# Performance work log

Measured on AMD Instinct MI355X. Metric: run time of the kernel, lower is better.

## Reference

```python
import jax, jax.numpy as jnp
import numpy as np

T, B = 80, 256                 # timesteps (max objs per image), num sequences (images)
OBJ_DIM, EMBED, HID = 4096, 200, 512
NCLS = 151                      # 150 VG classes + background
D = HID + OBJ_DIM + EMBED + 128 # decoder inputs_dim = 4936


def _packed_gather_idx():
    # descending lengths 80..41, mimicking a sorted PackedSequence
    lengths = np.array([T - (i * 40) // B for i in range(B)])
    idx = []
    for t in range(T):
        bs = int((lengths > t).sum())
        idx.extend(t * B + b for b in range(bs))
    return np.asarray(idx, dtype=np.int32)  # [15504]


def setup_inputs() -> dict:
    key = jax.random.key(0)
    ks = jax.random.split(key, 6)
    s = jnp.float32(0.02)
    return {
        "sequence": jax.random.normal(ks[0], (T, B, D), jnp.float32),
        "embed": jax.random.normal(ks[1], (NCLS + 1, EMBED), jnp.float32) * s,
        "W_in": jax.random.normal(ks[2], (6 * HID, D + EMBED), jnp.float32) * s,
        "b_in": jnp.zeros((6 * HID,), jnp.float32),
        "W_state": jax.random.normal(ks[3], (5 * HID, HID), jnp.float32) * s,
        "b_state": jnp.zeros((5 * HID,), jnp.float32),
        "W_out": jax.random.normal(ks[4], (NCLS, HID), jnp.float32) * s,
        "b_out": jnp.zeros((NCLS,), jnp.float32),
        "gather_idx": jnp.asarray(_packed_gather_idx()),
    }


def reference(sequence, embed, W_in, b_in, W_state, b_state, W_out, b_out, gather_idx):
    H = HID

    def step(carry, x_t):
        h, c, prev_embed = carry
        ti = jnp.concatenate([x_t, prev_embed], axis=1)          # [B, D+E]
        pi = ti @ W_in.T + b_in                                   # [B, 6H]
        ps = h @ W_state.T + b_state                              # [B, 5H]
        i_g = jax.nn.sigmoid(pi[:, 0*H:1*H] + ps[:, 0*H:1*H])
        f_g = jax.nn.sigmoid(pi[:, 1*H:2*H] + ps[:, 1*H:2*H])
        m_i = jnp.tanh(pi[:, 2*H:3*H] + ps[:, 2*H:3*H])
        o_g = jax.nn.sigmoid(pi[:, 3*H:4*H] + ps[:, 3*H:4*H])
        c_new = i_g * m_i + f_g * c
        out = o_g * jnp.tanh(c_new)
        hw_g = jax.nn.sigmoid(pi[:, 4*H:5*H] + ps[:, 4*H:5*H])
        h_new = hw_g * out + (1.0 - hw_g) * pi[:, 5*H:6*H]        # highway
        pred = h_new @ W_out.T + b_out                            # [B, NCLS]
        # softmax is monotonic: argmax of softmax(pred)[:,1:] == argmax of pred[:,1:]
        best = jnp.argmax(pred[:, 1:], axis=1) + 1                # [B], in [1, NCLS-1]
        pe_new = embed[best + 1]                                  # [B, E]
        return (h_new, c_new, pe_new), (pred, best)

    h0 = jnp.zeros((B, HID), sequence.dtype)
    c0 = jnp.zeros((B, HID), sequence.dtype)
    pe0 = jnp.broadcast_to(embed[0], (B, EMBED))                  # 'start' token embed
    _, (dists, commits) = jax.lax.scan(step, (h0, c0, pe0), sequence)
    # packed (timestep-major) flattening of valid entries only
    out_dists = dists.reshape(T * B, NCLS)[gather_idx]            # [N, NCLS]
    out_commits = commits.reshape(T * B)[gather_idx]              # [N]
    return out_dists, out_commits
```

## Files before the change

### kernel.cpp

```cpp
#include <hip/hip_runtime.h>
#include <cstddef>
#include <cstdint>

#define T_STEPS 80
#define BATCH   256
#define DIM     4936
#define EMB     200
#define DE      5136
#define HID     512
#define SIXH    3072
#define FIVEH   2560
#define NCLS    151
#define NPACK   15504
#define NKT     156
#define NKT_H   16
#define NCOMB   2816
#define BUF2SZ  32768
#define PSBUF   32768

typedef unsigned short ushort_t;
typedef short short8 __attribute__((ext_vector_type(8)));
typedef float f32x4 __attribute__((ext_vector_type(4)));
typedef float f32x16 __attribute__((ext_vector_type(16)));

__device__ inline ushort_t f2bf_rn(float x) {
    union { float f; uint32_t u; } v; v.f = x;
    uint32_t u = v.u;
    return (ushort_t)((u + 0x7FFFu + ((u >> 16) & 1u)) >> 16);
}
__device__ inline float bf2f(ushort_t b) {
    union { float f; uint32_t u; } v; v.u = ((uint32_t)b) << 16;
    return v.f;
}
__device__ inline float sigmoidf(float x) { return 1.f / (1.f + expf(-x)); }

__global__ __launch_bounds__(256) void convert_split(
    const float* __restrict__ src, int ld, int kvalid,
    ushort_t* __restrict__ hi, ushort_t* __restrict__ lo, int nktiles)
{
    __shared__ float s[128][33];
    const int tid = threadIdx.x;
    const int kt  = blockIdx.x;
    const int mt  = blockIdx.y;

#pragma unroll
    for (int it = 0; it < 4; ++it) {
        int idx = it * 256 + tid;
        int row = idx >> 3;
        int f4  = idx & 7;
        int k   = kt * 32 + f4 * 4;
        const float* p = src + (size_t)(mt * 128 + row) * ld + k;
        float4 v;
        if (k + 3 < kvalid) v = *(const float4*)p;
        else {
            v.x = (k + 0) < kvalid ? p[0] : 0.f;
            v.y = (k + 1) < kvalid ? p[1] : 0.f;
            v.z = (k + 2) < kvalid ? p[2] : 0.f;
            v.w = (k + 3) < kvalid ? p[3] : 0.f;
        }
        s[row][f4 * 4 + 0] = v.x; s[row][f4 * 4 + 1] = v.y;
        s[row][f4 * 4 + 2] = v.z; s[row][f4 * 4 + 3] = v.w;
    }
    __syncthreads();

    const size_t base = ((size_t)mt * nktiles + kt) * 4096;
#pragma unroll
    for (int it = 0; it < 2; ++it) {
        int o   = it * 256 + tid;
        int kb  = o >> 7;
        int row = o & 127;
        alignas(16) ushort_t hbuf[8];
        alignas(16) ushort_t lbuf[8];
#pragma unroll
        for (int e = 0; e < 8; ++e) {
            float x = s[row][kb * 8 + e];
            ushort_t hh = f2bf_rn(x);
            float lof = x - bf2f(hh);
            hbuf[e] = hh;
            lbuf[e] = f2bf_rn(lof);
        }
        *(uint4*)(hi + base + (size_t)o * 8) = *(const uint4*)hbuf;
        *(uint4*)(lo + base + (size_t)o * 8) = *(const uint4*)lbuf;
    }
}

__device__ inline void gload16(const ushort_t* g, ushort_t* l) {
    __builtin_amdgcn_global_load_lds(
        (const __attribute__((address_space(1))) void*)g,
        (__attribute__((address_space(3))) void*)l, 16, 0, 0);
}

__global__ __launch_bounds__(512, 1) void mfma3(
    const ushort_t* __restrict__ Ah, const ushort_t* __restrict__ Al,
    const ushort_t* __restrict__ Bh, const ushort_t* __restrict__ Bl,
    const float* __restrict__ bias, float* __restrict__ OUT,
    int nkt, int ldout, int nt)
{
    extern __shared__ __align__(16) ushort_t smem[];

    const int tid  = threadIdx.x;
    const int wave = tid >> 6;
    const int lane = tid & 63;

    int mtb, ntb;
    {
        const int L = blockIdx.x;
        if ((nt & 7) == 0) {
            const int x = L & 7;
            const int s = L >> 3;
            mtb = x + 8 * (s / 12);
            ntb = s % 12;
        } else {
            mtb = L / 12;
            ntb = L % 12;
        }
    }
    const int wr = wave >> 2;
    const int wc = wave & 3;

    f32x16 acc[4][2];
#pragma unroll
    for (int i = 0; i < 4; ++i)
#pragma unroll
        for (int j = 0; j < 2; ++j)
#pragma unroll
            for (int r = 0; r < 16; ++r) acc[i][j][r] = 0.f;

    const size_t a0 = (size_t)(2 * mtb) * nkt * 4096;
    const size_t a1 = a0 + (size_t)nkt * 4096;
    const size_t b0 = (size_t)(2 * ntb) * nkt * 4096;
    const size_t b1 = b0 + (size_t)nkt * 4096;

#define STAGE2(slot, kt_) do {                                      \
        ushort_t* d = smem + (slot) * BUF2SZ;                       \
        const size_t ko = (size_t)(kt_) * 4096 + tid * 8;           \
        gload16(Ah + a0 + ko, d + tid * 8);                         \
        gload16(Ah + a1 + ko, d + 4096 + tid * 8);                  \
        gload16(Al + a0 + ko, d + 8192 + tid * 8);                  \
        gload16(Al + a1 + ko, d + 12288 + tid * 8);                 \
        gload16(Bh + b0 + ko, d + 16384 + tid * 8);                 \
        gload16(Bh + b1 + ko, d + 20480 + tid * 8);                 \
        gload16(Bl + b0 + ko, d + 24576 + tid * 8);                 \
        gload16(Bl + b1 + ko, d + 28672 + tid * 8);                 \
    } while (0)

    const int lrow = lane & 31;
    const int kg   = lane >> 5;
    const int aBase = wr * 4096;
    const int bBase = 16384 + (wc >> 1) * 4096;
    const int bCol  = (wc & 1) * 64;

    STAGE2(0, 0);

    for (int kt = 0; kt < nkt; ++kt) {
        asm volatile("s_waitcnt vmcnt(0)" ::: "memory");
        __builtin_amdgcn_sched_barrier(0);
        __builtin_amdgcn_s_barrier();
        if (kt + 1 < nkt) STAGE2((kt + 1) & 1, kt + 1);

        const ushort_t* p = smem + (kt & 1) * BUF2SZ;
#pragma unroll
        for (int kh = 0; kh < 2; ++kh) {
            const int ko = (kh * 2 + kg) * 1024;
            short8 a_h[4], a_l[4], b_h[2], b_l[2];
#pragma unroll
            for (int ms = 0; ms < 4; ++ms) {
                const int ao = aBase + ko + (ms * 32 + lrow) * 8;
                a_h[ms] = *(const short8*)&p[ao];
                a_l[ms] = *(const short8*)&p[8192 + ao];
            }
#pragma unroll
            for (int ns = 0; ns < 2; ++ns) {
                const int bo = bBase + ko + (bCol + ns * 32 + lrow) * 8;
                b_h[ns] = *(const short8*)&p[bo];
                b_l[ns] = *(const short8*)&p[8192 + bo];
            }
#pragma unroll
            for (int ms = 0; ms < 4; ++ms)
#pragma unroll
                for (int ns = 0; ns < 2; ++ns) {
                    acc[ms][ns] = __builtin_amdgcn_mfma_f32_32x32x16_bf16(a_h[ms], b_h[ns], acc[ms][ns], 0, 0, 0);
                    acc[ms][ns] = __builtin_amdgcn_mfma_f32_32x32x16_bf16(a_h[ms], b_l[ns], acc[ms][ns], 0, 0, 0);
                    acc[ms][ns] = __builtin_amdgcn_mfma_f32_32x32x16_bf16(a_l[ms], b_h[ns], acc[ms][ns], 0, 0, 0);
                }
        }
    }
#undef STAGE2

#pragma unroll
    for (int ms = 0; ms < 4; ++ms)
#pragma unroll
        for (int ns = 0; ns < 2; ++ns) {
            const int col = ntb * 256 + wc * 64 + ns * 32 + (lane & 31);
            const float bv = bias[col];
            const int rowb = mtb * 256 + wr * 128 + ms * 32 + 4 * (lane >> 5);
#pragma unroll
            for (int r = 0; r < 16; ++r) {
                const int row = rowb + (r & 3) + 8 * (r >> 2);
                OUT[(size_t)row * ldout + col] = acc[ms][ns][r] + bv;
            }
        }
}

__global__ __launch_bounds__(256, 1) void ps_full(
    const ushort_t* __restrict__ hH, const ushort_t* __restrict__ hL,
    const ushort_t* __restrict__ WcH, const ushort_t* __restrict__ WcL,
    const float* __restrict__ bias_comb,
    float* __restrict__ psF)
{
    extern __shared__ __align__(16) ushort_t psmem[];

    const int tid  = threadIdx.x;
    const int wave = tid >> 6;
    const int lane = tid & 63;
    const int ntile = blockIdx.x;
    const int mtile = blockIdx.y;
    const int amt = mtile >> 1, arh = mtile & 1;
    const int bmt = ntile >> 1, brh = ntile & 1;
    const int wr = wave >> 1, wc = wave & 1;

    f32x4 acc[2][2];
#pragma unroll
    for (int i = 0; i < 2; ++i)
#pragma unroll
        for (int j = 0; j < 2; ++j) acc[i][j] = (f32x4){0.f, 0.f, 0.f, 0.f};

    const int lw    = wave * 512;
    const int lsrcA = wave * 1024 + arh * 512 + lane * 8;
    const int lsrcB = wave * 1024 + brh * 512 + lane * 8;
    const int kb = lane >> 4;
    const int lr = lane & 15;

#define STAGE_PS(slot, r_) do {                                           \
        ushort_t* d = psmem + (slot) * PSBUF;                             \
        _Pragma("unroll")                                                 \
        for (int ki_ = 0; ki_ < 4; ++ki_) {                               \
            const int kt_ = (r_) * 4 + ki_;                               \
            const size_t at_ = ((size_t)(amt * NKT_H + kt_)) * 4096;      \
            const size_t bt_ = ((size_t)(bmt * NKT_H + kt_)) * 4096;      \
            gload16(hH  + at_ + lsrcA, d + ki_ * 2048 + lw);              \
            gload16(hL  + at_ + lsrcA, d + 8192 + ki_ * 2048 + lw);       \
            gload16(WcH + bt_ + lsrcB, d + 16384 + ki_ * 2048 + lw);      \
            gload16(WcL + bt_ + lsrcB, d + 24576 + ki_ * 2048 + lw);      \
        }                                                                 \
    } while (0)

    STAGE_PS(0, 0);

    for (int r = 0; r < 4; ++r) {
        asm volatile("s_waitcnt vmcnt(0)" ::: "memory");
        __builtin_amdgcn_sched_barrier(0);
        __builtin_amdgcn_s_barrier();
        if (r + 1 < 4) STAGE_PS((r + 1) & 1, r + 1);

        const ushort_t* p = psmem + (r & 1) * PSBUF;
#pragma unroll
        for (int ki = 0; ki < 4; ++ki) {
            short8 ah[2], al[2], bh[2], bl[2];
#pragma unroll
            for (int i = 0; i < 2; ++i) {
                const int ao = ki * 2048 + kb * 512 + (wr * 32 + i * 16 + lr) * 8;
                ah[i] = *(const short8*)&p[ao];
                al[i] = *(const short8*)&p[8192 + ao];
            }
#pragma unroll
            for (int j = 0; j < 2; ++j) {
                const int bo = ki * 2048 + kb * 512 + (wc * 32 + j * 16 + lr) * 8;
                bh[j] = *(const short8*)&p[16384 + bo];
                bl[j] = *(const short8*)&p[24576 + bo];
            }
#pragma unroll
            for (int i = 0; i < 2; ++i)
#pragma unroll
                for (int j = 0; j < 2; ++j) {
                    acc[i][j] = __builtin_amdgcn_mfma_f32_16x16x32_bf16(ah[i], bh[j], acc[i][j], 0, 0, 0);
                    acc[i][j] = __builtin_amdgcn_mfma_f32_16x16x32_bf16(ah[i], bl[j], acc[i][j], 0, 0, 0);
                    acc[i][j] = __builtin_amdgcn_mfma_f32_16x16x32_bf16(al[i], bh[j], acc[i][j], 0, 0, 0);
                }
        }
    }
#undef STAGE_PS

    float* out = psF + (size_t)(mtile * 64) * NCOMB + ntile * 64;
#pragma unroll
    for (int i = 0; i < 2; ++i) {
        const int row = wr * 32 + i * 16 + (lane >> 4) * 4;
#pragma unroll
        for (int j = 0; j < 2; ++j) {
            const int col = wc * 32 + j * 16 + (lane & 15);
            const float bv = bias_comb[ntile * 64 + col];
#pragma unroll
            for (int r = 0; r < 4; ++r)
                out[(size_t)(row + r) * NCOMB + col] = acc[i][j][r] + bv;
        }
    }
}

__global__ __launch_bounds__(256) void ew_gemm(
    const float* __restrict__ embed, const float* __restrict__ Win,
    float* __restrict__ EW)
{
    __shared__ float As[16][68];
    __shared__ float Bs[16][68];
    const int tid = threadIdx.x;
    const int tx  = tid & 15;
    const int ty  = tid >> 4;
    const int n0  = blockIdx.x * 64;
    const int m0  = blockIdx.y * 64;
    const int lrow = tid >> 2;
    const int lk   = (tid & 3) * 4;

    float acc[4][4];
#pragma unroll
    for (int i = 0; i < 4; ++i)
#pragma unroll
        for (int j = 0; j < 4; ++j) acc[i][j] = 0.f;

    for (int k0 = 0; k0 < EMB; k0 += 16) {
        int k = k0 + lk;
        float4 av = {0.f,0.f,0.f,0.f}, bv = {0.f,0.f,0.f,0.f};
        if (k < EMB) {
            int am = m0 + lrow;
            if (am < 152) av = *(const float4*)(embed + (size_t)am * EMB + k);
            bv = *(const float4*)(Win + (size_t)(n0 + lrow) * DE + DIM + k);
        }
        __syncthreads();
        As[lk + 0][lrow] = av.x; As[lk + 1][lrow] = av.y;
        As[lk + 2][lrow] = av.z; As[lk + 3][lrow] = av.w;
        Bs[lk + 0][lrow] = bv.x; Bs[lk + 1][lrow] = bv.y;
        Bs[lk + 2][lrow] = bv.z; Bs[lk + 3][lrow] = bv.w;
        __syncthreads();
#pragma unroll
        for (int kk = 0; kk < 16; ++kk) {
            float4 a4 = *(const float4*)&As[kk][ty * 4];
            float4 b4 = *(const float4*)&Bs[kk][tx * 4];
            float avr[4] = {a4.x, a4.y, a4.z, a4.w};
            float bvr[4] = {b4.x, b4.y, b4.z, b4.w};
#pragma unroll
            for (int i = 0; i < 4; ++i)
#pragma unroll
                for (int j = 0; j < 4; ++j)
                    acc[i][j] = fmaf(avr[i], bvr[j], acc[i][j]);
        }
    }
#pragma unroll
    for (int i = 0; i < 4; ++i) {
        int m = m0 + ty * 4 + i;
        if (m < 152) {
#pragma unroll
            for (int j = 0; j < 4; ++j)
                EW[(size_t)m * SIXH + n0 + tx * 4 + j] = acc[i][j];
        }
    }
}

__global__ __launch_bounds__(256) void prep_misc(
    const float* __restrict__ Wout, const float* __restrict__ b_state,
    const float* __restrict__ b_out,
    float* __restrict__ padW, float* __restrict__ bc)
{
    int i = blockIdx.x * 256 + threadIdx.x;
    if (i < 256 * 512) {
        int row = i >> 9;
        padW[i] = (row < NCLS) ? Wout[i] : 0.f;
    }
    if (i < NCOMB) {
        float v;
        if (i < FIVEH)                 v = b_state[i];
        else if (i - FIVEH < NCLS)     v = b_out[i - FIVEH];
        else                           v = 0.f;
        bc[i] = v;
    }
}

__global__ __launch_bounds__(256) void init_state(
    float* __restrict__ c, ushort_t* __restrict__ hHt, ushort_t* __restrict__ hLt)
{
    int i = blockIdx.x * 256 + threadIdx.x;
    if (i < BATCH * HID) { c[i] = 0.f; hHt[i] = 0; hLt[i] = 0; }
}

__global__ __launch_bounds__(256) void step_fused(
    const float* __restrict__ px_t,
    const float* __restrict__ EW,
    const float* __restrict__ psF,
    int first,
    ushort_t* __restrict__ hHt, ushort_t* __restrict__ hLt,
    float* __restrict__ c, float* __restrict__ hF,
    float* __restrict__ dists_prev,
    int*   __restrict__ commit_prev)
{
    __shared__ float hs[HID];
    __shared__ float preds_s[NCLS + 1];
    __shared__ int   commit_sh;

    const int tid = threadIdx.x;
    const int b   = blockIdx.x;

    const float* px = px_t + (size_t)b * SIXH;
    const float* pp = psF + (size_t)b * NCOMB;

    float pxv[2][6], ppv[2][5], cv[2];
#pragma unroll
    for (int it = 0; it < 2; ++it) {
        const int u = it * 256 + tid;
#pragma unroll
        for (int k2 = 0; k2 < 5; ++k2) {
            pxv[it][k2] = px[k2 * HID + u];
            ppv[it][k2] = pp[k2 * HID + u];
        }
        pxv[it][5] = px[5 * HID + u];
        cv[it] = c[(size_t)b * HID + u];
    }

    int erow = 0;
    if (!first) {
        if (tid < NCLS) {
            float pr = pp[2560 + tid];
            preds_s[tid] = pr;
            dists_prev[(size_t)b * NCLS + tid] = pr;
        }
        __syncthreads();
        if (tid < 64) {
            float bv = -__builtin_inff();
            int   bi = NCLS;
            for (int n = 1 + tid; n < NCLS; n += 64) {
                float v = preds_s[n];
                if (v > bv) { bv = v; bi = n; }
            }
#pragma unroll
            for (int off = 32; off; off >>= 1) {
                float ov = __shfl_down(bv, off);
                int   oi = __shfl_down(bi, off);
                if (ov > bv || (ov == bv && oi < bi)) { bv = ov; bi = oi; }
            }
            if (tid == 0) {
                commit_prev[b] = bi;
                commit_sh = bi;
            }
        }
        __syncthreads();
        erow = commit_sh + 1;
    }

    const float* ew = EW + (size_t)erow * SIXH;

#pragma unroll
    for (int it = 0; it < 2; ++it) {
        const int u = it * 256 + tid;
        float p[6];
#pragma unroll
        for (int k2 = 0; k2 < 5; ++k2)
            p[k2] = pxv[it][k2] + ew[k2 * HID + u] + ppv[it][k2];
        p[5] = pxv[it][5] + ew[5 * HID + u];

        float i_g = sigmoidf(p[0]);
        float f_g = sigmoidf(p[1]);
        float m_i = tanhf(p[2]);
        float o_g = sigmoidf(p[3]);
        float c_new = i_g * m_i + f_g * cv[it];
        float outv  = o_g * tanhf(c_new);
        float hw    = sigmoidf(p[4]);
        float h_new = hw * outv + (1.f - hw) * p[5];
        c[(size_t)b * HID + u]  = c_new;
        hF[(size_t)b * HID + u] = h_new;
        hs[u] = h_new;
    }
    __syncthreads();

    if (tid < 128) {
        const int half = tid >> 6;
        const int ch   = tid & 63;
        const int mt   = b >> 7;
        const int row  = b & 127;
        const size_t off = ((size_t)(mt * NKT_H + (ch >> 2))) * 4096
                         + (size_t)(ch & 3) * 1024 + (size_t)row * 8;
        alignas(16) ushort_t buf[8];
        if (half == 0) {
#pragma unroll
            for (int e = 0; e < 8; ++e) buf[e] = f2bf_rn(hs[ch * 8 + e]);
            *(uint4*)(hHt + off) = *(const uint4*)buf;
        } else {
#pragma unroll
            for (int e = 0; e < 8; ++e) {
                float x = hs[ch * 8 + e];
                buf[e] = f2bf_rn(x - bf2f(f2bf_rn(x)));
            }
            *(uint4*)(hLt + off) = *(const uint4*)buf;
        }
    }
}

__global__ __launch_bounds__(192) void finalize_last(
    const float* __restrict__ hF, const float* __restrict__ Wout,
    const float* __restrict__ b_out,
    float* __restrict__ dists_last, int* __restrict__ commits_last)
{
    __shared__ float hsh[HID];
    __shared__ float preds[NCLS + 1];
    const int b = blockIdx.x;
    const int tid = threadIdx.x;

    if (tid < 128) {
        float4 v = *(const float4*)(hF + (size_t)b * HID + tid * 4);
        *(float4*)&hsh[tid * 4] = v;
    }
    __syncthreads();
    if (tid < NCLS) {
        const float* w = Wout + (size_t)tid * HID;
        float s0 = 0.f, s1 = 0.f, s2 = 0.f, s3 = 0.f;
        for (int k = 0; k < HID; k += 4) {
            float4 w4 = *(const float4*)(w + k);
            float4 h4 = *(const float4*)&hsh[k];
            s0 = fmaf(h4.x, w4.x, s0);
            s1 = fmaf(h4.y, w4.y, s1);
            s2 = fmaf(h4.z, w4.z, s2);
            s3 = fmaf(h4.w, w4.w, s3);
        }
        float s = b_out[tid] + ((s0 + s1) + (s2 + s3));
        preds[tid] = s;
        dists_last[(size_t)b * NCLS + tid] = s;
    }
    __syncthreads();
    if (tid == 0) {
        int bi = 1; float bv = preds[1];
        for (int n = 2; n < NCLS; ++n) {
            float v = preds[n];
            if (v > bv) { bv = v; bi = n; }
        }
        commits_last[b] = bi;
    }
}

__global__ __launch_bounds__(192) void gather_out(
    const float* __restrict__ dists, const int* __restrict__ commits,
    const int* __restrict__ gidx, float* __restrict__ out)
{
    const int i = blockIdx.x;
    const int g = gidx[i];
    if (threadIdx.x < NCLS)
        out[(size_t)i * NCLS + threadIdx.x] = dists[(size_t)g * NCLS + threadIdx.x];
    if (threadIdx.x == NCLS)
        out[(size_t)NPACK * NCLS + i] = (float)commits[g];
}

extern "C" void kernel_launch(void* const* d_in, const int* in_sizes, int n_in,
                              void* d_out, int out_size, void* d_ws, size_t ws_size,
                              hipStream_t stream)
{
    const float* X      = (const float*)d_in[0];
    const float* embed  = (const float*)d_in[1];
    const float* Win    = (const float*)d_in[2];
    const float* b_in   = (const float*)d_in[3];
    const float* Wst    = (const float*)d_in[4];
    const float* b_st   = (const float*)d_in[5];
    const float* Wout   = (const float*)d_in[6];
    const float* b_out  = (const float*)d_in[7];
    const int*   gidx   = (const int*)d_in[8];

    hipFuncSetAttribute((const void*)mfma3,
                        hipFuncAttributeMaxDynamicSharedMemorySize,
                        2 * BUF2SZ * 2);
    hipFuncSetAttribute((const void*)ps_full,
                        hipFuncAttributeMaxDynamicSharedMemorySize,
                        2 * PSBUF * 2);

    const size_t WN  = (size_t)24 * NKT * 4096;
    const size_t WCN = (size_t)22 * NKT_H * 4096;
    const size_t HN  = (size_t)2 * NKT_H * 4096;

    ushort_t* Wh  = (ushort_t*)d_ws;
    ushort_t* Wl  = Wh + WN;
    ushort_t* WcH = Wl + WN;
    ushort_t* WcL = WcH + WCN;
    ushort_t* hHt = WcL + WCN;
    ushort_t* hLt = hHt + HN;
    float* EW      = (float*)(hLt + HN);
    float* psF     = EW + (size_t)152 * SIXH;
    float* bc      = psF + (size_t)BATCH * NCOMB;
    float* c       = bc + NCOMB;
    float* hF      = c + (size_t)BATCH * HID;
    float* padW    = hF + (size_t)BATCH * HID;
    float* dists   = padW + (size_t)256 * HID;
    int* commits   = (int*)(dists + (size_t)T_STEPS * BATCH * NCLS);
    char* cbase    = (char*)(commits + T_STEPS * BATCH);

    size_t off = (size_t)(cbase - (char*)d_ws);
    off = (off + 255) & ~(size_t)255;
    const size_t per_t = (size_t)2 * 2 * NKT * 4096 * 2 + (size_t)BATCH * SIXH * 4;
    size_t rem = (ws_size > off) ? (ws_size - off) : 0;
    int CT = (int)(rem / per_t);
    if (CT > T_STEPS) CT = T_STEPS;
    if (CT < 1) CT = 1;

    ushort_t* Xh = (ushort_t*)((char*)d_ws + off);
    ushort_t* Xl = Xh + (size_t)2 * CT * NKT * 4096;
    float* px    = (float*)(Xl + (size_t)2 * CT * NKT * 4096);

    convert_split<<<dim3(NKT, 24), 256, 0, stream>>>(Win, DE, DIM, Wh, Wl, NKT);
    convert_split<<<dim3(NKT_H, 20), 256, 0, stream>>>(Wst, HID, HID, WcH, WcL, NKT_H);
    prep_misc<<<512, 256, 0, stream>>>(Wout, b_st, b_out, padW, bc);
    convert_split<<<dim3(NKT_H, 2), 256, 0, stream>>>(
        padW, HID, HID, WcH + (size_t)20 * NKT_H * 4096, WcL + (size_t)20 * NKT_H * 4096, NKT_H);
    ew_gemm<<<dim3(SIXH / 64, 3), 256, 0, stream>>>(embed, Win, EW);
    init_state<<<512, 256, 0, stream>>>(c, hHt, hLt);

    for (int t0 = 0; t0 < T_STEPS; t0 += CT) {
        int nt = T_STEPS - t0;
        if (nt > CT) nt = CT;
        convert_split<<<dim3(NKT, 2 * nt), 256, 0, stream>>>(
            X + (size_t)t0 * BATCH * DIM, DIM, DIM, Xh, Xl, NKT);
        mfma3<<<dim3((SIXH / 256) * nt), 512, 2 * BUF2SZ * 2, stream>>>(
            Xh, Xl, Wh, Wl, b_in, px, NKT, SIXH, nt);
        for (int t = t0; t < t0 + nt; ++t) {
            const int tp = (t > 0) ? t - 1 : 0;
            ps_full<<<dim3(44, 4), 256, 2 * PSBUF * 2, stream>>>(
                hHt, hLt, WcH, WcL, bc, psF);
            step_fused<<<BATCH, 256, 0, stream>>>(
                px + (size_t)(t - t0) * BATCH * SIXH, EW, psF,
                (t == 0) ? 1 : 0, hHt, hLt, c, hF,
                dists + (size_t)tp * BATCH * NCLS, commits + (size_t)tp * BATCH);
        }
    }

    finalize_last<<<BATCH, 192, 0, stream>>>(
        hF, Wout, b_out,
        dists + (size_t)(T_STEPS - 1) * BATCH * NCLS,
        commits + (size_t)(T_STEPS - 1) * BATCH);

    gather_out<<<NPACK, 192, 0, stream>>>(dists, commits, gidx, (float*)d_out);
}
```

Baseline: 2.901 ms.

## Fuse fp32-to-bf16 hi/lo split of input activations into the GEMM A-tile load

The separate convert_split pass over the input sequence is removed. The big input-projection GEMM now reads fp32 activations directly, splits them into bf16 hi/lo in registers, and writes them into shared memory. The split writes for the next tile happen between the two k-halves so they overlap with MFMA work. This removes a full read-write pass over the large activation tensor and frees workspace so larger time chunks fit. In exchange the GEMM carries more VALU conversion work and register pressure, and the reads re-fetch the fp32 rows across the 12 N-tiles.

```diff
diff --git a/kernel.cpp b/kernel.cpp
--- a/kernel.cpp
+++ b/kernel.cpp
@@ -91,7 +91,7 @@
 }
 
 __global__ __launch_bounds__(512, 1) void mfma3(
-    const ushort_t* __restrict__ Ah, const ushort_t* __restrict__ Al,
+    const float* __restrict__ Xsrc,
     const ushort_t* __restrict__ Bh, const ushort_t* __restrict__ Bl,
     const float* __restrict__ bias, float* __restrict__ OUT,
     int nkt, int ldout, int nt)
@@ -126,22 +126,53 @@
 #pragma unroll
             for (int r = 0; r < 16; ++r) acc[i][j][r] = 0.f;
 
-    const size_t a0 = (size_t)(2 * mtb) * nkt * 4096;
-    const size_t a1 = a0 + (size_t)nkt * 4096;
     const size_t b0 = (size_t)(2 * ntb) * nkt * 4096;
     const size_t b1 = b0 + (size_t)nkt * 4096;
 
-#define STAGE2(slot, kt_) do {                                      \
-        ushort_t* d = smem + (slot) * BUF2SZ;                       \
-        const size_t ko = (size_t)(kt_) * 4096 + tid * 8;           \
-        gload16(Ah + a0 + ko, d + tid * 8);                         \
-        gload16(Ah + a1 + ko, d + 4096 + tid * 8);                  \
-        gload16(Al + a0 + ko, d + 8192 + tid * 8);                  \
-        gload16(Al + a1 + ko, d + 12288 + tid * 8);                 \
-        gload16(Bh + b0 + ko, d + 16384 + tid * 8);                 \
-        gload16(Bh + b1 + ko, d + 20480 + tid * 8);                 \
-        gload16(Bl + b0 + ko, d + 24576 + tid * 8);                 \
-        gload16(Bl + b1 + ko, d + 28672 + tid * 8);                 \
+    const int arow = tid & 127;
+    const int akb  = tid >> 7;
+    const size_t xr0 = (size_t)(mtb * 256 + arow) * DIM;
+    const size_t xr1 = xr0 + (size_t)128 * DIM;
+
+    float4 fa0, fb0, fa1, fb1;
+
+#define LOADA(kt_) do {                                              \
+        const int k_ = (kt_) * 32 + akb * 8;                         \
+        if (k_ < DIM) {                                              \
+            const float* p0_ = Xsrc + xr0 + k_;                      \
+            const float* p1_ = Xsrc + xr1 + k_;                      \
+            fa0 = *(const float4*)p0_; fb0 = *(const float4*)(p0_ + 4); \
+            fa1 = *(const float4*)p1_; fb1 = *(const float4*)(p1_ + 4); \
+        } else {                                                     \
+            fa0 = fb0 = fa1 = fb1 = (float4){0.f, 0.f, 0.f, 0.f};    \
+        }                                                            \
+    } while (0)
+
+#define WRITEA(slot) do {                                            \
+        ushort_t* d_ = smem + (slot) * BUF2SZ;                       \
+        float t0_[8] = {fa0.x, fa0.y, fa0.z, fa0.w, fb0.x, fb0.y, fb0.z, fb0.w}; \
+        float t1_[8] = {fa1.x, fa1.y, fa1.z, fa1.w, fb1.x, fb1.y, fb1.z, fb1.w}; \
+        alignas(16) ushort_t h0_[8], l0_[8], h1_[8], l1_[8];         \
+        _Pragma("unroll")                                            \
+        for (int e_ = 0; e_ < 8; ++e_) {                             \
+            ushort_t hh_ = f2bf_rn(t0_[e_]);                         \
+            h0_[e_] = hh_; l0_[e_] = f2bf_rn(t0_[e_] - bf2f(hh_));   \
+            ushort_t hg_ = f2bf_rn(t1_[e_]);                         \
+            h1_[e_] = hg_; l1_[e_] = f2bf_rn(t1_[e_] - bf2f(hg_));   \
+        }                                                            \
+        *(uint4*)(d_ + tid * 8)         = *(const uint4*)h0_;        \
+        *(uint4*)(d_ + 4096 + tid * 8)  = *(const uint4*)h1_;        \
+        *(uint4*)(d_ + 8192 + tid * 8)  = *(const uint4*)l0_;        \
+        *(uint4*)(d_ + 12288 + tid * 8) = *(const uint4*)l1_;        \
+    } while (0)
+
+#define STAGE_B(slot, kt_) do {                                      \
+        ushort_t* d_ = smem + (slot) * BUF2SZ;                       \
+        const size_t ko_ = (size_t)(kt_) * 4096 + tid * 8;           \
+        gload16(Bh + b0 + ko_, d_ + 16384 + tid * 8);                \
+        gload16(Bh + b1 + ko_, d_ + 20480 + tid * 8);                \
+        gload16(Bl + b0 + ko_, d_ + 24576 + tid * 8);                \
+        gload16(Bl + b1 + ko_, d_ + 28672 + tid * 8);                \
     } while (0)
 
     const int lrow = lane & 31;
@@ -150,18 +181,23 @@
     const int bBase = 16384 + (wc >> 1) * 4096;
     const int bCol  = (wc & 1) * 64;
 
-    STAGE2(0, 0);
+    LOADA(0);
+    STAGE_B(0, 0);
+    WRITEA(0);
 
     for (int kt = 0; kt < nkt; ++kt) {
-        asm volatile("s_waitcnt vmcnt(0)" ::: "memory");
+        asm volatile("s_waitcnt vmcnt(0) lgkmcnt(0)" ::: "memory");
         __builtin_amdgcn_sched_barrier(0);
         __builtin_amdgcn_s_barrier();
-        if (kt + 1 < nkt) STAGE2((kt + 1) & 1, kt + 1);
+        const bool pre = (kt + 1 < nkt);
+        if (pre) {
+            STAGE_B((kt + 1) & 1, kt + 1);
+            LOADA(kt + 1);
+        }
 
         const ushort_t* p = smem + (kt & 1) * BUF2SZ;
-#pragma unroll
-        for (int kh = 0; kh < 2; ++kh) {
-            const int ko = (kh * 2 + kg) * 1024;
+        {
+            const int ko = kg * 1024;
             short8 a_h[4], a_l[4], b_h[2], b_l[2];
 #pragma unroll
             for (int ms = 0; ms < 4; ++ms) {
@@ -184,8 +220,35 @@
                     acc[ms][ns] = __builtin_amdgcn_mfma_f32_32x32x16_bf16(a_l[ms], b_h[ns], acc[ms][ns], 0, 0, 0);
                 }
         }
-    }
-#undef STAGE2
+        if (pre) WRITEA((kt + 1) & 1);
+        {
+            const int ko = (2 + kg) * 1024;
+            short8 a_h[4], a_l[4], b_h[2], b_l[2];
+#pragma unroll
+            for (int ms = 0; ms < 4; ++ms) {
+                const int ao = aBase + ko + (ms * 32 + lrow) * 8;
+                a_h[ms] = *(const short8*)&p[ao];
+                a_l[ms] = *(const short8*)&p[8192 + ao];
+            }
+#pragma unroll
+            for (int ns = 0; ns < 2; ++ns) {
+                const int bo = bBase + ko + (bCol + ns * 32 + lrow) * 8;
+                b_h[ns] = *(const short8*)&p[bo];
+                b_l[ns] = *(const short8*)&p[8192 + bo];
+            }
+#pragma unroll
+            for (int ms = 0; ms < 4; ++ms)
+#pragma unroll
+                for (int ns = 0; ns < 2; ++ns) {
+                    acc[ms][ns] = __builtin_amdgcn_mfma_f32_32x32x16_bf16(a_h[ms], b_h[ns], acc[ms][ns], 0, 0, 0);
+                    acc[ms][ns] = __builtin_amdgcn_mfma_f32_32x32x16_bf16(a_h[ms], b_l[ns], acc[ms][ns], 0, 0, 0);
+                    acc[ms][ns] = __builtin_amdgcn_mfma_f32_32x32x16_bf16(a_l[ms], b_h[ns], acc[ms][ns], 0, 0, 0);
+                }
+        }
+    }
+#undef LOADA
+#undef WRITEA
+#undef STAGE_B
 
 #pragma unroll
     for (int ms = 0; ms < 4; ++ms)
@@ -587,15 +650,13 @@
 
     size_t off = (size_t)(cbase - (char*)d_ws);
     off = (off + 255) & ~(size_t)255;
-    const size_t per_t = (size_t)2 * 2 * NKT * 4096 * 2 + (size_t)BATCH * SIXH * 4;
+    const size_t per_t = (size_t)BATCH * SIXH * 4;
     size_t rem = (ws_size > off) ? (ws_size - off) : 0;
     int CT = (int)(rem / per_t);
     if (CT > T_STEPS) CT = T_STEPS;
     if (CT < 1) CT = 1;
 
-    ushort_t* Xh = (ushort_t*)((char*)d_ws + off);
-    ushort_t* Xl = Xh + (size_t)2 * CT * NKT * 4096;
-    float* px    = (float*)(Xl + (size_t)2 * CT * NKT * 4096);
+    float* px = (float*)((char*)d_ws + off);
 
     convert_split<<<dim3(NKT, 24), 256, 0, stream>>>(Win, DE, DIM, Wh, Wl, NKT);
     convert_split<<<dim3(NKT_H, 20), 256, 0, stream>>>(Wst, HID, HID, WcH, WcL, NKT_H);
@@ -608,10 +669,8 @@
     for (int t0 = 0; t0 < T_STEPS; t0 += CT) {
         int nt = T_STEPS - t0;
         if (nt > CT) nt = CT;
-        convert_split<<<dim3(NKT, 2 * nt), 256, 0, stream>>>(
-            X + (size_t)t0 * BATCH * DIM, DIM, DIM, Xh, Xl, NKT);
         mfma3<<<dim3((SIXH / 256) * nt), 512, 2 * BUF2SZ * 2, stream>>>(
-            Xh, Xl, Wh, Wl, b_in, px, NKT, SIXH, nt);
+            X + (size_t)t0 * BATCH * DIM, Wh, Wl, b_in, px, NKT, SIXH, nt);
         for (int t = t0; t < t0 + nt; ++t) {
             const int tp = (t > 0) ? t - 1 : 0;
             ps_full<<<dim3(44, 4), 256, 2 * PSBUF * 2, stream>>>(
```

After: 3.124 ms. +7.7%, slower.
